# Kernel optimization log

Measured on AMD Instinct MI355X. Metric: run time of the kernel, lower is better.

## Reference

```python
import jax, jax.numpy as jnp
import numpy as np

B, N_O, N_Q = 2, 512, 512
POS_DIM, LATENT, HEADS, HEAD_DIM, OUT_DIM = 3, 256, 8, 32, 128
HD = HEADS * HEAD_DIM  # == LATENT here


def _lin(key, fan_in, fan_out):
    return jax.random.normal(key, (fan_in, fan_out), jnp.float32) / np.sqrt(fan_in)


def setup_inputs() -> dict:
    key = jax.random.key(0)
    ks = jax.random.split(key, 12)
    return {
        'h_obs': jax.random.normal(ks[0], (B, N_O, LATENT), jnp.float32),
        'pos_obs': jax.random.uniform(ks[1], (B, N_O, POS_DIM), jnp.float32),
        'pos_query': jax.random.uniform(ks[2], (B, N_Q, POS_DIM), jnp.float32),
        'fw1': _lin(ks[3], LATENT, LATENT), 'fb1': jnp.zeros((LATENT,), jnp.float32),
        'fw2': _lin(ks[4], LATENT, HD), 'fb2': jnp.zeros((HD,), jnp.float32),
        'log_sigma': jnp.zeros((HEADS,), jnp.float32),
        'kw1': _lin(ks[5], POS_DIM * 3, LATENT), 'kb1': jnp.zeros((LATENT,), jnp.float32),
        'kw2': _lin(ks[6], LATENT, HEADS), 'kb2': jnp.zeros((HEADS,), jnp.float32),
        'ow': _lin(ks[7], HD, OUT_DIM), 'ob': jnp.zeros((OUT_DIM,), jnp.float32),
        'vw': _lin(ks[8], HD, OUT_DIM), 'vb': jnp.zeros((OUT_DIM,), jnp.float32),
    }


def reference(h_obs, pos_obs, pos_query, fw1, fb1, fw2, fb2, log_sigma,
              kw1, kb1, kw2, kb2, ow, ob, vw, vb):
    Bv, No, _ = h_obs.shape
    Nq = pos_query.shape[1]
    # feature net -> values [B, H, N_o, D]
    v = jax.nn.relu(h_obs @ fw1 + fb1) @ fw2 + fb2
    v = v.reshape(Bv, No, HEADS, HEAD_DIM).transpose(0, 2, 1, 3)
    # pairwise relative positions [B, Nq, No, P]
    pos_q = pos_query[:, :, None, :]
    pos_o = pos_obs[:, None, :, :]
    rel = pos_q - pos_o
    dist2 = jnp.sum(rel ** 2, axis=-1)  # [B, Nq, No]
    sigma = jnp.exp(log_sigma)[None, :, None, None]
    rbf = jnp.exp(-dist2[:, None] / (sigma ** 2 + 1e-6))  # [B, H, Nq, No]
    # kernel MLP on concatenated pairwise positions [B, Nq, No, 3P] -> [B, H, Nq, No]
    ki = jnp.concatenate([
        jnp.broadcast_to(pos_q, (Bv, Nq, No, POS_DIM)),
        jnp.broadcast_to(pos_o, (Bv, Nq, No, POS_DIM)),
        rel], axis=-1)
    delta = (jax.nn.relu(ki @ kw1 + kb1) @ kw2 + kb2).transpose(0, 3, 1, 2)
    logits = jnp.log(rbf + 1e-8) + delta
    weights = jax.nn.softmax(logits, axis=-1)  # [B, H, Nq, No]
    # weighted mean over observations
    v_mean = jnp.einsum('bhqo,bhod->bhqd', weights, v)  # [B, H, Nq, D]
    h_query = v_mean.transpose(0, 2, 1, 3).reshape(Bv, Nq, HD)
    # weighted variance: sum_o w * (v_o - v_mean)^2
    residual = v[:, :, None, :, :] - v_mean[:, :, :, None, :]  # [B, H, Nq, No, D]
    var = jnp.sum(weights[..., None] * residual ** 2, axis=3)  # [B, H, Nq, D]
    var = var.transpose(0, 2, 1, 3).reshape(Bv, Nq, HD)
    mean = h_query @ ow + ob
    var_out = jax.nn.softplus(var @ vw + vb)
    return (mean, var_out)
```

## Files before the change

kernel.cpp:

```cpp
#include <hip/hip_runtime.h>
#include <math.h>

#define NB 2
#define NO 512
#define NQ 512
#define OUT_DIM 128
#define LPAD 516

typedef __attribute__((ext_vector_type(8))) _Float16 half8;
typedef __attribute__((ext_vector_type(4))) _Float16 half4;
typedef __attribute__((ext_vector_type(4))) float f32x4;

__device__ __forceinline__ float softplus_f(float x) {
  return x > 0.0f ? x + log1pf(expf(-x)) : log1pf(expf(x));
}
__device__ __forceinline__ half8 splat8(_Float16 v) {
  return (half8){v, v, v, v, v, v, v, v};
}
__device__ __forceinline__ half8 fma8(half8 a, half8 b, half8 c) {
  return __builtin_elementwise_fma(a, b, c);
}
__device__ __forceinline__ half8 max8(half8 a, half8 b) {
  return __builtin_elementwise_max(a, b);
}
__device__ __forceinline__ void gll16(const void* g, void* l) {
  __builtin_amdgcn_global_load_lds(
      (const __attribute__((address_space(1))) unsigned int*)g,
      (__attribute__((address_space(3))) unsigned int*)l, 16, 0, 0);
}

__global__ __launch_bounds__(1024) void prep_kernel(
    const float* __restrict__ h_obs, const float* __restrict__ fw1,
    const float* __restrict__ fb1, const float* __restrict__ fw2,
    const float* __restrict__ fb2, _Float16* __restrict__ VT)
{
  __shared__ float s_red[4][4][256];
  __shared__ float s_hid[4][256];
  const int n  = threadIdx.x & 255;
  const int ks = threadIdx.x >> 8;
  const int r0 = blockIdx.x * 4;
  const int k0 = ks * 64;
  float a0 = 0.f, a1 = 0.f, a2 = 0.f, a3 = 0.f;
  #pragma unroll 8
  for (int kk = 0; kk < 64; ++kk) {
    int k = k0 + kk;
    float w = fw1[k * 256 + n];
    a0 = fmaf(h_obs[(r0 + 0) * 256 + k], w, a0);
    a1 = fmaf(h_obs[(r0 + 1) * 256 + k], w, a1);
    a2 = fmaf(h_obs[(r0 + 2) * 256 + k], w, a2);
    a3 = fmaf(h_obs[(r0 + 3) * 256 + k], w, a3);
  }
  s_red[ks][0][n] = a0; s_red[ks][1][n] = a1;
  s_red[ks][2][n] = a2; s_red[ks][3][n] = a3;
  __syncthreads();
  if (ks == 0) {
    float bb = fb1[n];
    #pragma unroll
    for (int r = 0; r < 4; ++r) {
      float v = s_red[0][r][n] + s_red[1][r][n] + s_red[2][r][n] + s_red[3][r][n] + bb;
      s_hid[r][n] = fmaxf(v, 0.f);
    }
  }
  __syncthreads();
  float c0 = 0.f, c1 = 0.f, c2 = 0.f, c3 = 0.f;
  #pragma unroll 8
  for (int kk = 0; kk < 64; ++kk) {
    int k = k0 + kk;
    float w = fw2[k * 256 + n];
    c0 = fmaf(s_hid[0][k], w, c0);
    c1 = fmaf(s_hid[1][k], w, c1);
    c2 = fmaf(s_hid[2][k], w, c2);
    c3 = fmaf(s_hid[3][k], w, c3);
  }
  __syncthreads();
  s_red[ks][0][n] = c0; s_red[ks][1][n] = c1;
  s_red[ks][2][n] = c2; s_red[ks][3][n] = c3;
  __syncthreads();
  if (ks == 0) {
    float bb = fb2[n];
    float vr[4];
    #pragma unroll
    for (int r = 0; r < 4; ++r)
      vr[r] = s_red[0][r][n] + s_red[1][r][n] + s_red[2][r][n] + s_red[3][r][n] + bb;
    const int h  = n >> 5, d = n & 31;
    const int bb_ = r0 >> 9, o0 = r0 & 511;
    half4 pv;
    #pragma unroll
    for (int r = 0; r < 4; ++r) pv[r] = (_Float16)vr[r];
    *(half4*)(VT + ((size_t)((bb_ * 8 + h) * 32 + d)) * 512 + o0) = pv;
  }
}

__global__ __launch_bounds__(512, 4) void attn_fused(
    const _Float16* __restrict__ VT,
    const float* __restrict__ kw1,
    const float* __restrict__ kb1,
    const float* __restrict__ kw2,
    const float* __restrict__ kb2,
    const float* __restrict__ log_sigma,
    const float* __restrict__ pos_obs,
    const float* __restrict__ pos_query,
    const float* __restrict__ ow, const float* __restrict__ obias,
    const float* __restrict__ vw, const float* __restrict__ vbias,
    float* __restrict__ out)
{
  __shared__ __align__(16) float s_logits[2][8 * LPAD];
  __shared__ __align__(16) _Float16 s_P16[2][8][520];
  __shared__ half8 s_Bh[512];
  __shared__ __align__(16) float s_pool[2048];
  __shared__ __align__(16) float s_po[3][516];
  __shared__ __align__(16) _Float16 s_co[3][264];

  _Float16* s_aq2 = (_Float16*)s_pool;
  float*    s_hv   = s_pool;
  float*    s_pred = s_pool + 1024;

  const int t   = threadIdx.x;
  const int bq0 = blockIdx.x * 2;
  const int b   = bq0 >> 9;

  float pqx[2], pqy[2], pqz[2];
  #pragma unroll
  for (int q = 0; q < 2; ++q) {
    pqx[q] = pos_query[(bq0 + q) * 3 + 0];
    pqy[q] = pos_query[(bq0 + q) * 3 + 1];
    pqz[q] = pos_query[(bq0 + q) * 3 + 2];
  }
  {
    const int q = t >> 8, j = t & 255;
    float c0 = kw1[0 * 256 + j] + kw1[6 * 256 + j];
    float c1 = kw1[1 * 256 + j] + kw1[7 * 256 + j];
    float c2 = kw1[2 * 256 + j] + kw1[8 * 256 + j];
    s_aq2[q * 256 + j] = (_Float16)
        fmaf(pqx[q], c0, fmaf(pqy[q], c1, fmaf(pqz[q], c2, kb1[j])));
  }
  if (t < 256) {
    const int j = t;
    s_co[0][j] = (_Float16)(kw1[3 * 256 + j] - kw1[6 * 256 + j]);
    s_co[1][j] = (_Float16)(kw1[4 * 256 + j] - kw1[7 * 256 + j]);
    s_co[2][j] = (_Float16)(kw1[5 * 256 + j] - kw1[8 * 256 + j]);
  }
  {
    const int o = t;
    const float* p = pos_obs + (size_t)(b * NO + o) * 3;
    float px = p[0], py = p[1], pz = p[2];
    s_po[0][o] = px; s_po[1][o] = py; s_po[2][o] = pz;
    float d2q[2];
    #pragma unroll
    for (int q = 0; q < 2; ++q) {
      float r0 = pqx[q] - px, r1 = pqy[q] - py, r2 = pqz[q] - pz;
      d2q[q] = r0 * r0 + r1 * r1 + r2 * r2;
    }
    #pragma unroll
    for (int h = 0; h < 8; ++h) {
      float sg  = __expf(log_sigma[h]);
      float inv = 1.0f / (sg * sg + 1e-6f);
      float kbv = kb2[h];
      s_logits[0][h * LPAD + o] = fmaxf(-d2q[0] * inv, -18.420681f) + kbv;
      s_logits[1][h * LPAD + o] = fmaxf(-d2q[1] * inv, -18.420681f) + kbv;
    }
  }
  {
    const int kstep = t >> 6, lane = t & 63;
    const int nh = lane & 15;
    const int kb_ = kstep * 32 + ((lane >> 4) & 3) * 8;
    half8 b8;
    #pragma unroll
    for (int i = 0; i < 8; ++i) {
      float v = (nh < 8) ? kw2[(kb_ + i) * 8 + nh] : 0.f;
      b8[i] = (_Float16)v;
    }
    s_Bh[kstep * 64 + lane] = b8;
  }
  __syncthreads();

  {
    const int wave = t >> 6, lane = t & 63;
    const int quad = lane >> 4, mrow = lane & 15;
    const int tb   = wave * 4;
    _Float16 pxh[4], pyh[4], pzh[4];
    #pragma unroll
    for (int jt = 0; jt < 4; ++jt) {
      const int o = (tb + jt) * 16 + mrow;
      pxh[jt] = (_Float16)s_po[0][o];
      pyh[jt] = (_Float16)s_po[1][o];
      pzh[jt] = (_Float16)s_po[2][o];
    }
    f32x4 C[2][4];
    #pragma unroll
    for (int q = 0; q < 2; ++q)
      #pragma unroll
      for (int jt = 0; jt < 4; ++jt) C[q][jt] = (f32x4){0.f, 0.f, 0.f, 0.f};

    const half8 z8 = {0, 0, 0, 0, 0, 0, 0, 0};
    #pragma unroll
    for (int kstep = 0; kstep < 8; ++kstep) {
      const int koff = kstep * 32 + quad * 8;
      half8 c0 = *(const half8*)&s_co[0][koff];
      half8 c1 = *(const half8*)&s_co[1][koff];
      half8 c2 = *(const half8*)&s_co[2][koff];
      half8 aq0 = *(const half8*)(s_aq2 + koff);
      half8 aq1 = *(const half8*)(s_aq2 + 256 + koff);
      half8 bh  = s_Bh[kstep * 64 + lane];
      #pragma unroll
      for (int jt = 0; jt < 4; ++jt) {
        half8 ao = fma8(splat8(pxh[jt]), c0,
                   fma8(splat8(pyh[jt]), c1, splat8(pzh[jt]) * c2));
        half8 a0 = max8(aq0 + ao, z8);
        half8 a1 = max8(aq1 + ao, z8);
        C[0][jt] = __builtin_amdgcn_mfma_f32_16x16x32_f16(a0, bh, C[0][jt], 0, 0, 0);
        C[1][jt] = __builtin_amdgcn_mfma_f32_16x16x32_f16(a1, bh, C[1][jt], 0, 0, 0);
      }
    }
    const int hh = lane & 15;
    if (hh < 8) {
      #pragma unroll
      for (int q = 0; q < 2; ++q)
        #pragma unroll
        for (int jt = 0; jt < 4; ++jt) {
          const int ob2 = (tb + jt) * 16 + quad * 4;
          #pragma unroll
          for (int r = 0; r < 4; ++r)
            s_logits[q][hh * LPAD + ob2 + r] += C[q][jt][r];
        }
    }
  }
  __syncthreads();

  {
    const int h = t >> 6, lane = t & 63;
    const int kg = lane >> 4, dl = lane & 15;
    char* stg0 = (char*)s_Bh + h * 1024;
    char* b1   = (char*)&s_logits[0][h * LPAD];
    char* b3   = b1 + 1024;
    char* b2   = (char*)&s_logits[1][h * LPAD];
    const int lp = lane ^ ((lane >> 3) & 1);
    const _Float16* vsrc = VT + ((size_t)(b * 8 + h) << 14)
                         + (lp >> 1) * 512 + (lp & 1) * 8;
    gll16(vsrc, stg0);

    float s0 = 0.f, s1 = 0.f;
    {
      const float* pl0 = &s_logits[0][h * LPAD] + lane * 8;
      const float* pl1 = &s_logits[1][h * LPAD] + lane * 8;
      half8 P0, P1;
      #pragma unroll
      for (int k = 0; k < 8; ++k) {
        float p0 = __expf(pl0[k] - 2.7725887f);
        float p1 = __expf(pl1[k] - 2.7725887f);
        s0 += p0; s1 += p1;
        P0[k] = (_Float16)p0;
        P1[k] = (_Float16)p1;
      }
      *(half8*)&s_P16[0][h][lane * 8] = P0;
      *(half8*)&s_P16[1][h][lane * 8] = P1;
    }
    gll16(vsrc + 16, b1);
    gll16(vsrc + 32, b2);
    gll16(vsrc + 48, b3);

    const int slot = ((kg & 1) ^ ((dl >> 2) & 1)) << 4;
    const char* pE = ((kg & 2) ? b1 : stg0) + dl * 32 + slot;
    const char* pO = ((kg & 2) ? b3 : b2)   + dl * 32 + slot;
    const _Float16* pB = &s_P16[lane & 1][h][0];
    f32x4 Cm0 = {0.f, 0.f, 0.f, 0.f}, Cm1 = Cm0, Cv0 = Cm0, Cv1 = Cm0;
    #pragma unroll
    for (int kp = 0; kp < 8; ++kp) {
      asm volatile("s_waitcnt vmcnt(2)" ::: "memory");
      {
        half8 am0 = *(const half8*)(pE);
        half8 am1 = *(const half8*)(pE + 512);
        half8 pb  = *(const half8*)(pB + (2 * kp) * 32 + kg * 8);
        half8 av0 = am0 * am0;
        half8 av1 = am1 * am1;
        __builtin_amdgcn_s_setprio(1);
        Cm0 = __builtin_amdgcn_mfma_f32_16x16x32_f16(am0, pb, Cm0, 0, 0, 0);
        Cm1 = __builtin_amdgcn_mfma_f32_16x16x32_f16(am1, pb, Cm1, 0, 0, 0);
        Cv0 = __builtin_amdgcn_mfma_f32_16x16x32_f16(av0, pb, Cv0, 0, 0, 0);
        Cv1 = __builtin_amdgcn_mfma_f32_16x16x32_f16(av1, pb, Cv1, 0, 0, 0);
        __builtin_amdgcn_s_setprio(0);
      }
      if (kp < 7) {
        asm volatile("s_waitcnt lgkmcnt(0)" ::: "memory");
        gll16(vsrc + (4 * kp + 4) * 16, stg0);
        gll16(vsrc + (4 * kp + 5) * 16, b1);
      }
      if (kp < 7) asm volatile("s_waitcnt vmcnt(2)" ::: "memory");
      else        asm volatile("s_waitcnt vmcnt(0)" ::: "memory");
      {
        half8 am0 = *(const half8*)(pO);
        half8 am1 = *(const half8*)(pO + 512);
        half8 pb  = *(const half8*)(pB + (2 * kp + 1) * 32 + kg * 8);
        half8 av0 = am0 * am0;
        half8 av1 = am1 * am1;
        __builtin_amdgcn_s_setprio(1);
        Cm0 = __builtin_amdgcn_mfma_f32_16x16x32_f16(am0, pb, Cm0, 0, 0, 0);
        Cm1 = __builtin_amdgcn_mfma_f32_16x16x32_f16(am1, pb, Cm1, 0, 0, 0);
        Cv0 = __builtin_amdgcn_mfma_f32_16x16x32_f16(av0, pb, Cv0, 0, 0, 0);
        Cv1 = __builtin_amdgcn_mfma_f32_16x16x32_f16(av1, pb, Cv1, 0, 0, 0);
        __builtin_amdgcn_s_setprio(0);
      }
      if (kp < 7) {
        asm volatile("s_waitcnt lgkmcnt(0)" ::: "memory");
        gll16(vsrc + (4 * kp + 6) * 16, b2);
        gll16(vsrc + (4 * kp + 7) * 16, b3);
      }
    }
    #pragma unroll
    for (int off = 32; off >= 1; off >>= 1) {
      s0 += __shfl_xor(s0, off, 64);
      s1 += __shfl_xor(s1, off, 64);
    }
    const int nq = lane & 15;
    if (nq < 2) {
      const float iv = 1.0f / (nq ? s1 : s0);
      const int dbase = h * 32 + kg * 4;
      f32x4 m0, v0, m1, v1;
      #pragma unroll
      for (int r = 0; r < 4; ++r) {
        float a = Cm0[r] * iv;
        m0[r] = a; v0[r] = fmaxf(Cv0[r] * iv - a * a, 0.f);
        float c = Cm1[r] * iv;
        m1[r] = c; v1[r] = fmaxf(Cv1[r] * iv - c * c, 0.f);
      }
      *(f32x4*)(s_hv + (nq * 2 + 0) * 256 + dbase)      = m0;
      *(f32x4*)(s_hv + (nq * 2 + 1) * 256 + dbase)      = v0;
      *(f32x4*)(s_hv + (nq * 2 + 0) * 256 + dbase + 16) = m1;
      *(f32x4*)(s_hv + (nq * 2 + 1) * 256 + dbase + 16) = v1;
    }
  }
  __syncthreads();

  {
    const int ks = t >> 8, mode = (t >> 7) & 1, n = t & 127;
    const float* W  = mode ? vw : ow;
    const float* X0 = s_hv + mode * 256;
    const float* X1 = s_hv + (2 + mode) * 256;
    float a0 = 0.f, a1 = 0.f;
    const int k0 = ks * 128;
    #pragma unroll 4
    for (int k = k0; k < k0 + 128; k += 4) {
      float4 x0 = *(const float4*)&X0[k];
      float4 x1 = *(const float4*)&X1[k];
      float w0 = W[(k + 0) * 128 + n];
      float w1 = W[(k + 1) * 128 + n];
      float w2 = W[(k + 2) * 128 + n];
      float w3 = W[(k + 3) * 128 + n];
      a0 = fmaf(x0.x, w0, a0); a1 = fmaf(x1.x, w0, a1);
      a0 = fmaf(x0.y, w1, a0); a1 = fmaf(x1.y, w1, a1);
      a0 = fmaf(x0.z, w2, a0); a1 = fmaf(x1.z, w2, a1);
      a0 = fmaf(x0.w, w3, a0); a1 = fmaf(x1.w, w3, a1);
    }
    s_pred[((ks * 2 + mode) * 2 + 0) * 128 + n] = a0;
    s_pred[((ks * 2 + mode) * 2 + 1) * 128 + n] = a1;
  }
  __syncthreads();
  {
    const int q = t >> 8, mode = (t >> 7) & 1, n = t & 127;
    float v = s_pred[((0 * 2 + mode) * 2 + q) * 128 + n]
            + s_pred[((1 * 2 + mode) * 2 + q) * 128 + n]
            + (mode ? vbias[n] : obias[n]);
    if (mode) v = softplus_f(v);
    out[(size_t)mode * (NB * NQ * OUT_DIM) + (size_t)(bq0 + q) * OUT_DIM + n] = v;
  }
}

extern "C" void kernel_launch(void* const* d_in, const int* in_sizes, int n_in,
                              void* d_out, int out_size, void* d_ws, size_t ws_size,
                              hipStream_t stream)
{
  const float* h_obs     = (const float*)d_in[0];
  const float* pos_obs   = (const float*)d_in[1];
  const float* pos_query = (const float*)d_in[2];
  const float* fw1       = (const float*)d_in[3];
  const float* fb1       = (const float*)d_in[4];
  const float* fw2       = (const float*)d_in[5];
  const float* fb2       = (const float*)d_in[6];
  const float* log_sigma = (const float*)d_in[7];
  const float* kw1       = (const float*)d_in[8];
  const float* kb1       = (const float*)d_in[9];
  const float* kw2       = (const float*)d_in[10];
  const float* kb2       = (const float*)d_in[11];
  const float* ow        = (const float*)d_in[12];
  const float* ob        = (const float*)d_in[13];
  const float* vw        = (const float*)d_in[14];
  const float* vb        = (const float*)d_in[15];

  float* out = (float*)d_out;
  _Float16* VT = (_Float16*)d_ws;

  prep_kernel<<<256, 1024, 0, stream>>>(h_obs, fw1, fb1, fw2, fb2, VT);
  attn_fused<<<NB * NQ / 2, 512, 0, stream>>>(VT, kw1, kb1, kw2, kb2,
                                              log_sigma, pos_obs, pos_query,
                                              ow, ob, vw, vb, out);
}
```

Baseline: 125.4 us.

## Deepen V staging pipeline to three buffer pairs with inline-asm LDS access

```diff
diff --git a/kernel.cpp b/kernel.cpp
--- a/kernel.cpp
+++ b/kernel.cpp
@@ -27,6 +27,9 @@
   __builtin_amdgcn_global_load_lds(
       (const __attribute__((address_space(1))) unsigned int*)g,
       (__attribute__((address_space(3))) unsigned int*)l, 16, 0, 0);
+}
+__device__ __forceinline__ unsigned as3(const void* p) {
+  return (unsigned)(unsigned long long)(const __attribute__((address_space(3))) char*)p;
 }
 
 __global__ __launch_bounds__(1024) void prep_kernel(
@@ -230,82 +233,110 @@
   {
     const int h = t >> 6, lane = t & 63;
     const int kg = lane >> 4, dl = lane & 15;
-    char* stg0 = (char*)s_Bh + h * 1024;
-    char* b1   = (char*)&s_logits[0][h * LPAD];
-    char* b3   = b1 + 1024;
-    char* b2   = (char*)&s_logits[1][h * LPAD];
+    char* B0 = (char*)s_Bh + h * 1024;
+    char* B1 = (h < 4) ? ((char*)s_pool + 4096 + h * 1024)
+                       : ((char*)s_po + (h - 4) * 1024);
+    char* B2 = (char*)&s_logits[0][h * LPAD];
+    char* B3 = B2 + 1024;
+    char* B4 = (char*)&s_logits[1][h * LPAD];
+    char* B5 = B4 + 1024;
     const int lp = lane ^ ((lane >> 3) & 1);
     const _Float16* vsrc = VT + ((size_t)(b * 8 + h) << 14)
                          + (lp >> 1) * 512 + (lp & 1) * 8;
-    gll16(vsrc, stg0);
-
+    gll16(vsrc + 0 * 16, B0);
+    gll16(vsrc + 1 * 16, B1);
+
+    unsigned l0A = as3(&s_logits[0][h * LPAD]) + lane * 32;
+    unsigned l1A = as3(&s_logits[1][h * LPAD]) + lane * 32;
+    int4 La, Lb, Lc, Ld;
+    asm volatile("ds_read_b128 %0, %4\n\t"
+                 "ds_read_b128 %1, %4 offset:16\n\t"
+                 "ds_read_b128 %2, %5\n\t"
+                 "ds_read_b128 %3, %5 offset:16\n\t"
+                 "s_waitcnt lgkmcnt(0)"
+                 : "=&v"(La), "=&v"(Lb), "=&v"(Lc), "=&v"(Ld)
+                 : "v"(l0A), "v"(l1A) : "memory");
+    f32x4 f0 = __builtin_bit_cast(f32x4, La);
+    f32x4 f1 = __builtin_bit_cast(f32x4, Lb);
+    f32x4 g0 = __builtin_bit_cast(f32x4, Lc);
+    f32x4 g1 = __builtin_bit_cast(f32x4, Ld);
     float s0 = 0.f, s1 = 0.f;
+    half8 P0, P1;
+    #pragma unroll
+    for (int k = 0; k < 4; ++k) {
+      float p0 = __expf(f0[k] - 2.7725887f);
+      float p1 = __expf(f1[k] - 2.7725887f);
+      float p2 = __expf(g0[k] - 2.7725887f);
+      float p3 = __expf(g1[k] - 2.7725887f);
+      s0 += p0 + p1; s1 += p2 + p3;
+      P0[k] = (_Float16)p0; P0[k + 4] = (_Float16)p1;
+      P1[k] = (_Float16)p2; P1[k + 4] = (_Float16)p3;
+    }
     {
-      const float* pl0 = &s_logits[0][h * LPAD] + lane * 8;
-      const float* pl1 = &s_logits[1][h * LPAD] + lane * 8;
-      half8 P0, P1;
-      #pragma unroll
-      for (int k = 0; k < 8; ++k) {
-        float p0 = __expf(pl0[k] - 2.7725887f);
-        float p1 = __expf(pl1[k] - 2.7725887f);
-        s0 += p0; s1 += p1;
-        P0[k] = (_Float16)p0;
-        P1[k] = (_Float16)p1;
-      }
-      *(half8*)&s_P16[0][h][lane * 8] = P0;
-      *(half8*)&s_P16[1][h][lane * 8] = P1;
-    }
-    gll16(vsrc + 16, b1);
-    gll16(vsrc + 32, b2);
-    gll16(vsrc + 48, b3);
+      int4 P0v = __builtin_bit_cast(int4, P0);
+      int4 P1v = __builtin_bit_cast(int4, P1);
+      unsigned p0A = as3(&s_P16[0][h][0]) + lane * 16;
+      unsigned p1A = as3(&s_P16[1][h][0]) + lane * 16;
+      asm volatile("ds_write2_b32 %0, %1, %2 offset0:0 offset1:1\n\t"
+                   "ds_write2_b32 %0, %3, %4 offset0:2 offset1:3\n\t"
+                   "ds_write2_b32 %5, %6, %7 offset0:0 offset1:1\n\t"
+                   "ds_write2_b32 %5, %8, %9 offset0:2 offset1:3"
+                   :: "v"(p0A), "v"(P0v.x), "v"(P0v.y), "v"(P0v.z), "v"(P0v.w),
+                      "v"(p1A), "v"(P1v.x), "v"(P1v.y), "v"(P1v.z), "v"(P1v.w)
+                   : "memory");
+    }
+    gll16(vsrc + 2 * 16, B2);
+    gll16(vsrc + 3 * 16, B3);
+    gll16(vsrc + 4 * 16, B4);
+    gll16(vsrc + 5 * 16, B5);
 
     const int slot = ((kg & 1) ^ ((dl >> 2) & 1)) << 4;
-    const char* pE = ((kg & 2) ? b1 : stg0) + dl * 32 + slot;
-    const char* pO = ((kg & 2) ? b3 : b2)   + dl * 32 + slot;
-    const _Float16* pB = &s_P16[lane & 1][h][0];
+    const unsigned amP0 = as3((kg < 2) ? B0 : B1) + dl * 32 + slot;
+    const unsigned amP1 = as3((kg < 2) ? B2 : B3) + dl * 32 + slot;
+    const unsigned amP2 = as3((kg < 2) ? B4 : B5) + dl * 32 + slot;
+    const unsigned pbA  = as3(&s_P16[lane & 1][h][0]) + kg * 16;
+
     f32x4 Cm0 = {0.f, 0.f, 0.f, 0.f}, Cm1 = Cm0, Cv0 = Cm0, Cv1 = Cm0;
-    #pragma unroll
-    for (int kp = 0; kp < 8; ++kp) {
-      asm volatile("s_waitcnt vmcnt(2)" ::: "memory");
-      {
-        half8 am0 = *(const half8*)(pE);
-        half8 am1 = *(const half8*)(pE + 512);
-        half8 pb  = *(const half8*)(pB + (2 * kp) * 32 + kg * 8);
-        half8 av0 = am0 * am0;
-        half8 av1 = am1 * am1;
-        __builtin_amdgcn_s_setprio(1);
-        Cm0 = __builtin_amdgcn_mfma_f32_16x16x32_f16(am0, pb, Cm0, 0, 0, 0);
-        Cm1 = __builtin_amdgcn_mfma_f32_16x16x32_f16(am1, pb, Cm1, 0, 0, 0);
-        Cv0 = __builtin_amdgcn_mfma_f32_16x16x32_f16(av0, pb, Cv0, 0, 0, 0);
-        Cv1 = __builtin_amdgcn_mfma_f32_16x16x32_f16(av1, pb, Cv1, 0, 0, 0);
-        __builtin_amdgcn_s_setprio(0);
-      }
-      if (kp < 7) {
-        asm volatile("s_waitcnt lgkmcnt(0)" ::: "memory");
-        gll16(vsrc + (4 * kp + 4) * 16, stg0);
-        gll16(vsrc + (4 * kp + 5) * 16, b1);
-      }
-      if (kp < 7) asm volatile("s_waitcnt vmcnt(2)" ::: "memory");
-      else        asm volatile("s_waitcnt vmcnt(0)" ::: "memory");
-      {
-        half8 am0 = *(const half8*)(pO);
-        half8 am1 = *(const half8*)(pO + 512);
-        half8 pb  = *(const half8*)(pB + (2 * kp + 1) * 32 + kg * 8);
-        half8 av0 = am0 * am0;
-        half8 av1 = am1 * am1;
-        __builtin_amdgcn_s_setprio(1);
-        Cm0 = __builtin_amdgcn_mfma_f32_16x16x32_f16(am0, pb, Cm0, 0, 0, 0);
-        Cm1 = __builtin_amdgcn_mfma_f32_16x16x32_f16(am1, pb, Cm1, 0, 0, 0);
-        Cv0 = __builtin_amdgcn_mfma_f32_16x16x32_f16(av0, pb, Cv0, 0, 0, 0);
-        Cv1 = __builtin_amdgcn_mfma_f32_16x16x32_f16(av1, pb, Cv1, 0, 0, 0);
-        __builtin_amdgcn_s_setprio(0);
-      }
-      if (kp < 7) {
-        asm volatile("s_waitcnt lgkmcnt(0)" ::: "memory");
-        gll16(vsrc + (4 * kp + 6) * 16, b2);
-        gll16(vsrc + (4 * kp + 7) * 16, b3);
-      }
-    }
+#define PVSTEP(s, AM, WN, REFILL)                                          \
+    { asm volatile("s_waitcnt vmcnt(" WN ")" ::: "memory");                \
+      int4 A0v, A1v, PBv;                                                  \
+      asm volatile("ds_read_b128 %0, %3\n\t"                               \
+                   "ds_read_b128 %1, %3 offset:512\n\t"                    \
+                   "ds_read_b128 %2, %4\n\t"                               \
+                   "s_waitcnt lgkmcnt(0)"                                  \
+                   : "=&v"(A0v), "=&v"(A1v), "=&v"(PBv)                    \
+                   : "v"(AM), "v"(pbA + (s) * 64)                          \
+                   : "memory");                                            \
+      half8 am0 = __builtin_bit_cast(half8, A0v);                          \
+      half8 am1 = __builtin_bit_cast(half8, A1v);                          \
+      half8 pb  = __builtin_bit_cast(half8, PBv);                          \
+      half8 av0 = am0 * am0, av1 = am1 * am1;                              \
+      __builtin_amdgcn_s_setprio(1);                                       \
+      Cm0 = __builtin_amdgcn_mfma_f32_16x16x32_f16(am0, pb, Cm0, 0, 0, 0); \
+      Cm1 = __builtin_amdgcn_mfma_f32_16x16x32_f16(am1, pb, Cm1, 0, 0, 0); \
+      Cv0 = __builtin_amdgcn_mfma_f32_16x16x32_f16(av0, pb, Cv0, 0, 0, 0); \
+      Cv1 = __builtin_amdgcn_mfma_f32_16x16x32_f16(av1, pb, Cv1, 0, 0, 0); \
+      __builtin_amdgcn_s_setprio(0);                                       \
+      REFILL }
+
+    PVSTEP( 0, amP0, "4", gll16(vsrc +  6 * 16, B0); gll16(vsrc +  7 * 16, B1);)
+    PVSTEP( 1, amP1, "4", gll16(vsrc +  8 * 16, B2); gll16(vsrc +  9 * 16, B3);)
+    PVSTEP( 2, amP2, "4", gll16(vsrc + 10 * 16, B4); gll16(vsrc + 11 * 16, B5);)
+    PVSTEP( 3, amP0, "4", gll16(vsrc + 12 * 16, B0); gll16(vsrc + 13 * 16, B1);)
+    PVSTEP( 4, amP1, "4", gll16(vsrc + 14 * 16, B2); gll16(vsrc + 15 * 16, B3);)
+    PVSTEP( 5, amP2, "4", gll16(vsrc + 16 * 16, B4); gll16(vsrc + 17 * 16, B5);)
+    PVSTEP( 6, amP0, "4", gll16(vsrc + 18 * 16, B0); gll16(vsrc + 19 * 16, B1);)
+    PVSTEP( 7, amP1, "4", gll16(vsrc + 20 * 16, B2); gll16(vsrc + 21 * 16, B3);)
+    PVSTEP( 8, amP2, "4", gll16(vsrc + 22 * 16, B4); gll16(vsrc + 23 * 16, B5);)
+    PVSTEP( 9, amP0, "4", gll16(vsrc + 24 * 16, B0); gll16(vsrc + 25 * 16, B1);)
+    PVSTEP(10, amP1, "4", gll16(vsrc + 26 * 16, B2); gll16(vsrc + 27 * 16, B3);)
+    PVSTEP(11, amP2, "4", gll16(vsrc + 28 * 16, B4); gll16(vsrc + 29 * 16, B5);)
+    PVSTEP(12, amP0, "4", gll16(vsrc + 30 * 16, B0); gll16(vsrc + 31 * 16, B1);)
+    PVSTEP(13, amP1, "4", )
+    PVSTEP(14, amP2, "2", )
+    PVSTEP(15, amP0, "0", )
+#undef PVSTEP
+
     #pragma unroll
     for (int off = 32; off >= 1; off >>= 1) {
       s0 += __shfl_xor(s0, off, 64);
```

Measured after the change: 133.8 us. +6.6%, slower.
